# Kernel tuning notes

Hardware: AMD Instinct MI355X
Metric: run time of the kernel (lower is better)

The kernel has to match this reference:

```python
import jax, jax.numpy as jnp
import numpy as np

B, C, H, L, D = 128, 5, 50, 32, 300
VOCAB = 50000
KN = 20  # len(torch.arange(-0.9, 1.1, 0.1))
EPS = 1e-8


def setup_inputs() -> dict:
    key = jax.random.key(0)
    k1, k2, k3, k4 = jax.random.split(key, 4)
    return {
        "candidate_title": jax.random.randint(k1, (B, C, L), 0, VOCAB),
        "clicked_title": jax.random.randint(k2, (B, H, L), 0, VOCAB),
        "embedding": jax.random.normal(k3, (VOCAB, D), dtype=jnp.float32),
        "ltr_w": jax.random.normal(k4, (1, H * KN), dtype=jnp.float32) * 0.03,
        "ltr_b": jnp.zeros((1,), dtype=jnp.float32),
    }


def reference(candidate_title, clicked_title, embedding, ltr_w, ltr_b):
    mus = jnp.arange(KN, dtype=jnp.float32) * 0.1 - 0.9
    sigmas = jnp.concatenate([jnp.full((KN - 1,), 0.1, dtype=jnp.float32),
                              jnp.array([0.001], dtype=jnp.float32)])

    ce = embedding[candidate_title]            # [B,C,L,D]
    he = embedding[clicked_title]              # [B,H,L,D]
    # torch CosineSimilarity: dot / (clamp(||a||,eps)*clamp(||b||,eps))
    cn = ce / jnp.clip(jnp.linalg.norm(ce, axis=-1, keepdims=True), EPS)
    hn = he / jnp.clip(jnp.linalg.norm(he, axis=-1, keepdims=True), EPS)
    sim = jnp.einsum('bcid,bhjd->bchij', cn, hn)  # [B,C,H,L,L] fusion matrix

    # kernel pooling: sum over columns j per Gaussian kernel, then log-sum over rows i
    pooled = jnp.stack(
        [jnp.sum(jnp.exp(-(sim - mus[k]) ** 2 / (2.0 * sigmas[k] ** 2)), axis=-1)
         for k in range(KN)], axis=-1)          # [B,C,H,L,KN]
    pv = jnp.sum(jnp.log(jnp.clip(pooled, 1e-10)), axis=-2)  # [B,C,H,KN]
    pv = pv.reshape(B, C, H * KN)

    score = pv @ ltr_w.T + ltr_b               # [B,C,1]
    return jax.nn.log_softmax(score, axis=1)[..., 0]  # [B,C]
```

## Files before the change

kernel.cpp:

```cpp
#include <hip/hip_runtime.h>
#include <hip/hip_bf16.h>

#define VOCABN 50000
#define BN 128
#define CN 5
#define HN 50
#define LN 32
#define DN 300
#define DP 320
#define KNN 20

typedef __bf16    bf16x8 __attribute__((ext_vector_type(8)));
typedef float     f32x4  __attribute__((ext_vector_type(4)));
typedef float     f32x2  __attribute__((ext_vector_type(2)));
typedef ushort    u16x8  __attribute__((ext_vector_type(8)));

#if __has_builtin(__builtin_amdgcn_exp2f)
#define FEXP2 __builtin_amdgcn_exp2f
#else
#define FEXP2 exp2f
#endif
#if __has_builtin(__builtin_amdgcn_logf)
#define FLOG2 __builtin_amdgcn_logf
#else
#define FLOG2 log2f
#endif

#define LOG2E 1.4426950408889634f
#define LN2F  0.6931471805599453f

__global__ __launch_bounds__(256) void knorm_embed2(const float* __restrict__ emb,
                                                    ushort* __restrict__ tabo) {
    const int t    = threadIdx.x;
    const int lane = t & 63;
    const int w    = t >> 6;
    const int v    = blockIdx.x * 4 + w;
    const float* row = emb + (size_t)v * DN;
    const float4* r4 = (const float4*)row;

    float4 x = r4[lane];
    float ss = x.x * x.x + x.y * x.y + x.z * x.z + x.w * x.w;
    if (lane < 11) {
        float4 y = r4[64 + lane];
        ss += y.x * y.x + y.y * y.y + y.z * y.z + y.w * y.w;
    }
    #pragma unroll
    for (int off = 32; off; off >>= 1) ss += __shfl_xor(ss, off);
    const float scale = 1.0f / fmaxf(sqrtf(ss), 1e-8f);

    if (lane < 40) {
        u16x8 u;
        #pragma unroll
        for (int j = 0; j < 8; ++j) {
            int e = lane * 8 + j;
            float f = (e < DN) ? row[e] * scale : 0.f;
            __hip_bfloat16 h = __float2bfloat16(f);
            u[j] = *(ushort*)&h;
        }
        *(u16x8*)(tabo + (size_t)v * DP + lane * 8) = u;
    }
}

__device__ __forceinline__ int paddr(int row, int c) {
    return ((row >> 1) << 7) + ((((c + ((row & 1) << 2))) ^ ((row >> 1) & 7)) << 4);
}
__device__ __forceinline__ bf16x8 ldP(const ushort* buf, int row, int c) {
    return *(const bf16x8*)((const char*)buf + paddr(row, c));
}

__global__ __launch_bounds__(320, 6) void knrm_fused8(const int* __restrict__ cand,
                                                      const int* __restrict__ clik,
                                                      const ushort* __restrict__ tab,
                                                      const float* __restrict__ ltr_w,
                                                      float* __restrict__ score) {
    __shared__ __align__(16) char smem[25344];
    ushort* Abuf0 = (ushort*)smem;
    ushort* Abuf1 = (ushort*)(smem + 10240);
    ushort* Bbuf0 = (ushort*)(smem + 20480);
    ushort* Bbuf1 = (ushort*)(smem + 22528);
    int*    tokA  = (int*)(smem + 24576);
    int*    tokB  = (int*)(smem + 25216);

    const int t    = threadIdx.x;
    const int lane = t & 63;
    const int w    = t >> 6;
    const int bid  = (blockIdx.x & 7) * 800 + (blockIdx.x >> 3);
    const int b    = bid / HN;
    const int h    = bid % HN;

    if (t < 160)      tokA[t] = cand[b * (CN * LN) + t];
    else if (t < 192) tokB[t - 160] = clik[b * (HN * LN) + h * LN + (t - 160)];
    __syncthreads();

    const int m15 = lane & 15;
    const int g4  = lane >> 4;

    const char* srcA[2]; int dstA[2];
    #pragma unroll
    for (int it = 0; it < 2; ++it) {
        int cid = it * 320 + t, ar = cid >> 2, c = cid & 3;
        srcA[it] = (const char*)tab + (size_t)tokA[ar] * (DP * 2) + c * 16;
        dstA[it] = paddr(ar, c);
    }
    const char* srcB; int dstB;
    {
        int tb = t & 127;
        int ar = tb >> 2, c = tb & 3;
        srcB = (const char*)tab + (size_t)tokB[ar] * (DP * 2) + c * 16;
        dstB = paddr(ar, c);
    }

    f32x4 acc[2][2];
    #pragma unroll
    for (int at = 0; at < 2; ++at)
        #pragma unroll
        for (int jg = 0; jg < 2; ++jg)
            acc[at][jg] = (f32x4){0.f, 0.f, 0.f, 0.f};

    {
        int4 a0 = *(const int4*)(srcA[0]);
        int4 a1 = *(const int4*)(srcA[1]);
        int4 b0; if (t < 128) b0 = *(const int4*)(srcB);
        *(int4*)((char*)Abuf0 + dstA[0]) = a0;
        *(int4*)((char*)Abuf0 + dstA[1]) = a1;
        if (t < 128) *(int4*)((char*)Bbuf0 + dstB) = b0;
    }
    __syncthreads();

    #pragma unroll 2
    for (int ss = 0; ss < 10; ++ss) {
        const ushort* A = (ss & 1) ? Abuf1 : Abuf0;
        const ushort* B = (ss & 1) ? Bbuf1 : Bbuf0;

        int4 a0, a1, b0;
        if (ss < 9) {
            const int so = (ss + 1) * 64;
            a0 = *(const int4*)(srcA[0] + so);
            a1 = *(const int4*)(srcA[1] + so);
            if (t < 128) b0 = *(const int4*)(srcB + so);
        }

        bf16x8 af0 = ldP(A, w * 32 + m15,      g4);
        bf16x8 af1 = ldP(A, w * 32 + 16 + m15, g4);
        bf16x8 bf0 = ldP(B, m15,      g4);
        bf16x8 bf1 = ldP(B, 16 + m15, g4);
        acc[0][0] = __builtin_amdgcn_mfma_f32_16x16x32_bf16(af0, bf0, acc[0][0], 0, 0, 0);
        acc[0][1] = __builtin_amdgcn_mfma_f32_16x16x32_bf16(af0, bf1, acc[0][1], 0, 0, 0);
        acc[1][0] = __builtin_amdgcn_mfma_f32_16x16x32_bf16(af1, bf0, acc[1][0], 0, 0, 0);
        acc[1][1] = __builtin_amdgcn_mfma_f32_16x16x32_bf16(af1, bf1, acc[1][1], 0, 0, 0);

        if (ss < 9) {
            char* An = (char*)((ss & 1) ? Abuf0 : Abuf1);
            char* Bn = (char*)((ss & 1) ? Bbuf0 : Bbuf1);
            *(int4*)(An + dstA[0]) = a0;
            *(int4*)(An + dstA[1]) = a1;
            if (t < 128) *(int4*)(Bn + dstB) = b0;
            __syncthreads();
        }
    }
    __syncthreads();

    const float C1   = 10.0f * LOG2E;
    const float C2   = -50.0f * LOG2E;
    const float AK19 = 849.3218002880191f;
    static const float CkT[10] = {
        1.0f, 0.6065306597126334f, 0.1353352832366127f, 0.011108996538242306f,
        3.3546262790251185e-4f, 3.7266531720786709e-6f, 1.5229979744712628e-8f,
        2.2897348456191135e-11f, 1.2664165549094176e-14f, 2.576757109154981e-18f };

    float* sb = (float*)(smem + w * 4224);

    #pragma unroll
    for (int at = 0; at < 2; ++at)
        #pragma unroll
        for (int jgl = 0; jgl < 2; ++jgl)
            #pragma unroll
            for (int r = 0; r < 4; ++r)
                sb[(at * 16 + g4 * 4 + r) * 33 + jgl * 16 + m15] = acc[at][jgl][r];

    const int hi = lane >> 5;
    const float* sp = sb + (lane & 31) * 33 + hi * 16;

    f32x2 Qp[9];
    #pragma unroll
    for (int j = 0; j < 9; ++j) Qp[j] = (f32x2){0.f, 0.f};
    float Q9 = 0.f, Q19 = 0.f;

    #pragma unroll
    for (int ec = 0; ec < 4; ++ec) {
        f32x4 v = *(const f32x4*)(sp + ec * 4);
        #pragma unroll
        for (int e = 0; e < 4; ++e) {
            float s  = v[e];
            float cs = C1 * s;
            float tt = FEXP2(cs);
            float uu = FEXP2(-cs);
            float e0 = FEXP2(C2 * (s * s));
            Q9 += e0;
            f32x2 tu = {tt, uu};
            f32x2 pm = {e0, e0};
            #pragma unroll
            for (int j = 0; j < 9; ++j) { pm *= tu; Qp[j] += pm; }
            float d = fmaf(s, AK19, -AK19);
            Q19 += FEXP2(-(d * d));
        }
    }

    #pragma unroll
    for (int j = 0; j < 9; ++j) {
        Qp[j].x += __shfl_xor(Qp[j].x, 32);
        Qp[j].y += __shfl_xor(Qp[j].y, 32);
    }
    Q9  += __shfl_xor(Q9, 32);
    Q19 += __shfl_xor(Q19, 32);

    const float* wrow = ltr_w + h * KNN;
    float q0 = hi ? Q19 : Q9;
    float w0 = wrow[hi ? 19 : 9];
    float res = w0 * FLOG2(fmaxf(q0, 1e-10f));
    #pragma unroll
    for (int j = 1; j <= 9; ++j) {
        float q  = hi ? Qp[j - 1].x : Qp[j - 1].y;
        float wk = wrow[hi ? (9 + j) : (9 - j)];
        res += wk * FLOG2(fmaxf(q * CkT[j], 1e-10f));
    }

    res *= LN2F;
    #pragma unroll
    for (int off = 32; off; off >>= 1) res += __shfl_xor(res, off);
    if (lane == 0) atomicAdd(&score[b * CN + w], res);
}

__global__ __launch_bounds__(128) void knrm_final(const float* __restrict__ score,
                                                  float* __restrict__ out) {
    int b = threadIdx.x;
    if (b < BN) {
        float s[CN];
        float m = -1e30f;
        #pragma unroll
        for (int c = 0; c < CN; ++c) { s[c] = score[b * CN + c]; m = fmaxf(m, s[c]); }
        float sum = 0.f;
        #pragma unroll
        for (int c = 0; c < CN; ++c) sum += FEXP2((s[c] - m) * LOG2E);
        float lse = m + FLOG2(sum) * LN2F;
        #pragma unroll
        for (int c = 0; c < CN; ++c) out[b * CN + c] = s[c] - lse;
    }
}

extern "C" void kernel_launch(void* const* d_in, const int* in_sizes, int n_in,
                              void* d_out, int out_size, void* d_ws, size_t ws_size,
                              hipStream_t stream) {
    const int*   cand  = (const int*)d_in[0];
    const int*   clik  = (const int*)d_in[1];
    const float* emb   = (const float*)d_in[2];
    const float* ltr_w = (const float*)d_in[3];
    float* out = (float*)d_out;

    const size_t TAB_B = (size_t)VOCABN * DP * 2;

    ushort* tab  = (ushort*)d_ws;
    float*  scre = (float*)((char*)d_ws + TAB_B);

    hipMemsetAsync(scre, 0, BN * CN * sizeof(float), stream);
    knorm_embed2<<<VOCABN / 4, 256, 0, stream>>>(emb, tab);
    knrm_fused8<<<BN * HN, 320, 0, stream>>>(cand, clik, tab, ltr_w, scre);
    knrm_final<<<1, 128, 0, stream>>>(scre, out);
}
```

Measured before the change: 131.5 us.

## Load A fragments directly from global into registers, prefetch B two stages ahead

The candidate-side A operand is now read straight from global memory into MFMA fragment registers, and is no longer staged through LDS with double buffering. Each wave loads only its own rows. The B (clicked) tile is still staged in LDS but is now prefetched two stages ahead in registers. This removes LDS writes and reads for A and frees LDS space, in exchange for narrower 16-byte-per-lane global loads in fragment layout. Those loads may coalesce less well, and the deeper prefetch raises register pressure.

After: 144.4 us. +9.8%, slower.

```diff
diff --git a/kernel.cpp b/kernel.cpp
--- a/kernel.cpp
+++ b/kernel.cpp
@@ -68,18 +68,16 @@
     return *(const bf16x8*)((const char*)buf + paddr(row, c));
 }
 
-__global__ __launch_bounds__(320, 6) void knrm_fused8(const int* __restrict__ cand,
+__global__ __launch_bounds__(320, 6) void knrm_fused9(const int* __restrict__ cand,
                                                       const int* __restrict__ clik,
                                                       const ushort* __restrict__ tab,
                                                       const float* __restrict__ ltr_w,
                                                       float* __restrict__ score) {
-    __shared__ __align__(16) char smem[25344];
-    ushort* Abuf0 = (ushort*)smem;
-    ushort* Abuf1 = (ushort*)(smem + 10240);
-    ushort* Bbuf0 = (ushort*)(smem + 20480);
-    ushort* Bbuf1 = (ushort*)(smem + 22528);
-    int*    tokA  = (int*)(smem + 24576);
-    int*    tokB  = (int*)(smem + 25216);
+    __shared__ __align__(16) char smem[25984];
+    ushort* Bbuf0 = (ushort*)(smem + 21120);
+    ushort* Bbuf1 = (ushort*)(smem + 23168);
+    int*    tokA  = (int*)(smem + 25216);
+    int*    tokB  = (int*)(smem + 25856);
 
     const int t    = threadIdx.x;
     const int lane = t & 63;
@@ -95,13 +93,9 @@
     const int m15 = lane & 15;
     const int g4  = lane >> 4;
 
-    const char* srcA[2]; int dstA[2];
-    #pragma unroll
-    for (int it = 0; it < 2; ++it) {
-        int cid = it * 320 + t, ar = cid >> 2, c = cid & 3;
-        srcA[it] = (const char*)tab + (size_t)tokA[ar] * (DP * 2) + c * 16;
-        dstA[it] = paddr(ar, c);
-    }
+    const char* sA0 = (const char*)tab + (size_t)tokA[w * 32 + m15]      * (DP * 2) + g4 * 16;
+    const char* sA1 = (const char*)tab + (size_t)tokA[w * 32 + 16 + m15] * (DP * 2) + g4 * 16;
+
     const char* srcB; int dstB;
     {
         int tb = t & 127;
@@ -117,31 +111,27 @@
         for (int jg = 0; jg < 2; ++jg)
             acc[at][jg] = (f32x4){0.f, 0.f, 0.f, 0.f};
 
-    {
-        int4 a0 = *(const int4*)(srcA[0]);
-        int4 a1 = *(const int4*)(srcA[1]);
-        int4 b0; if (t < 128) b0 = *(const int4*)(srcB);
-        *(int4*)((char*)Abuf0 + dstA[0]) = a0;
-        *(int4*)((char*)Abuf0 + dstA[1]) = a1;
-        if (t < 128) *(int4*)((char*)Bbuf0 + dstB) = b0;
-    }
+    int4 bcur, bnext;
+    if (t < 128) {
+        int4 b0 = *(const int4*)(srcB);
+        *(int4*)((char*)Bbuf0 + dstB) = b0;
+        bcur = *(const int4*)(srcB + 64);
+    }
+    bf16x8 af0 = *(const bf16x8*)(sA0);
+    bf16x8 af1 = *(const bf16x8*)(sA1);
     __syncthreads();
 
     #pragma unroll 2
     for (int ss = 0; ss < 10; ++ss) {
-        const ushort* A = (ss & 1) ? Abuf1 : Abuf0;
         const ushort* B = (ss & 1) ? Bbuf1 : Bbuf0;
 
-        int4 a0, a1, b0;
+        if (ss < 8 && t < 128) bnext = *(const int4*)(srcB + (ss + 2) * 64);
+        bf16x8 an0 = af0, an1 = af1;
         if (ss < 9) {
-            const int so = (ss + 1) * 64;
-            a0 = *(const int4*)(srcA[0] + so);
-            a1 = *(const int4*)(srcA[1] + so);
-            if (t < 128) b0 = *(const int4*)(srcB + so);
-        }
-
-        bf16x8 af0 = ldP(A, w * 32 + m15,      g4);
-        bf16x8 af1 = ldP(A, w * 32 + 16 + m15, g4);
+            an0 = *(const bf16x8*)(sA0 + (ss + 1) * 64);
+            an1 = *(const bf16x8*)(sA1 + (ss + 1) * 64);
+        }
+
         bf16x8 bf0 = ldP(B, m15,      g4);
         bf16x8 bf1 = ldP(B, 16 + m15, g4);
         acc[0][0] = __builtin_amdgcn_mfma_f32_16x16x32_bf16(af0, bf0, acc[0][0], 0, 0, 0);
@@ -150,13 +140,11 @@
         acc[1][1] = __builtin_amdgcn_mfma_f32_16x16x32_bf16(af1, bf1, acc[1][1], 0, 0, 0);
 
         if (ss < 9) {
-            char* An = (char*)((ss & 1) ? Abuf0 : Abuf1);
-            char* Bn = (char*)((ss & 1) ? Bbuf0 : Bbuf1);
-            *(int4*)(An + dstA[0]) = a0;
-            *(int4*)(An + dstA[1]) = a1;
-            if (t < 128) *(int4*)(Bn + dstB) = b0;
+            if (t < 128) *(int4*)((char*)((ss & 1) ? Bbuf0 : Bbuf1) + dstB) = bcur;
             __syncthreads();
         }
+        af0 = an0; af1 = an1;
+        bcur = bnext;
     }
     __syncthreads();
 
@@ -264,6 +252,6 @@
 
     hipMemsetAsync(scre, 0, BN * CN * sizeof(float), stream);
     knorm_embed2<<<VOCABN / 4, 256, 0, stream>>>(emb, tab);
-    knrm_fused8<<<BN * HN, 320, 0, stream>>>(cand, clik, tab, ltr_w, scre);
+    knrm_fused9<<<BN * HN, 320, 0, stream>>>(cand, clik, tab, ltr_w, scre);
     knrm_final<<<1, 128, 0, stream>>>(scre, out);
 }
```
